# Performance work log

Hardware: AMD Instinct MI355X
Metric: run time of the kernel (lower is better)

The kernel has to match this reference:

```python
import jax, jax.numpy as jnp
import numpy as np

B, S, D, H = 4, 2048, 1024, 16
DK = D // H

def setup_inputs() -> dict:
    key = jax.random.key(0)
    ks = jax.random.split(key, 5)
    scale = 1.0 / np.sqrt(D)
    return {
        "x": jax.random.normal(ks[0], (B, S, D), dtype=jnp.float32),
        "Wq": jax.random.normal(ks[1], (H, D, DK), dtype=jnp.float32) * scale,
        "Wk": jax.random.normal(ks[2], (H, D, DK), dtype=jnp.float32) * scale,
        "Wv": jax.random.normal(ks[3], (H, D, DK), dtype=jnp.float32) * scale,
        "Wo": jax.random.normal(ks[4], (D, D), dtype=jnp.float32) * scale,
    }

def reference(x, Wq, Wk, Wv, Wo):
    # x: [B,S,D]; Wq/Wk/Wv: [H,D,DK] (stacked per-head Linear weights); Wo: [D,D]
    seq = x.shape[-2]
    q = jnp.einsum('bsd,hdk->bhsk', x, Wq)
    k = jnp.einsum('bsd,hdk->bhsk', x, Wk)
    v = jnp.einsum('bsd,hdk->bhsk', x, Wv)
    dk = q.shape[-1]
    scores = jnp.einsum('bhqk,bhsk->bhqs', q, k) / jnp.sqrt(jnp.asarray(dk, x.dtype))
    # causal mask: mask out strictly-future positions (triu, diagonal=1)
    causal = jnp.tril(jnp.ones((seq, seq), dtype=bool))  # True = keep
    scores = jnp.where(causal, scores, -jnp.inf)
    probs = jax.nn.softmax(scores, axis=-1)  # attn_pdrop = 0.0 -> dropout is identity
    attn = jnp.einsum('bhqs,bhsk->bhqk', probs, v)
    # concat heads: [B,S,H*DK]
    concat = attn.transpose(0, 2, 1, 3).reshape(x.shape[0], seq, -1)
    # output_proj: nn.Linear(D, D, bias=False) -> y = concat @ Wo.T
    return jnp.einsum('bsd,ed->bse', concat, Wo)
```

## Files before the change

kernel.cpp:

```cpp
#include <hip/hip_runtime.h>
#include <hip/hip_bf16.h>

#define B_ 4
#define S_ 2048
#define D_ 1024
#define H_ 16
#define DK_ 64

typedef __attribute__((ext_vector_type(8))) short bf16x8;
typedef __attribute__((ext_vector_type(4))) float f32x4;
typedef __attribute__((ext_vector_type(4))) unsigned int u32x4;

__device__ __forceinline__ unsigned short f2bf(float f) {
    unsigned int u = __float_as_uint(f);
    u += 0x7FFFu + ((u >> 16) & 1u);
    return (unsigned short)(u >> 16);
}

__device__ __forceinline__ unsigned int cvtpk_bf16(float lo, float hi) {
    unsigned int r;
    asm("v_cvt_pk_bf16_f32 %0, %1, %2" : "=v"(r) : "v"(lo), "v"(hi));
    return r;
}

#define BAR() do { __builtin_amdgcn_s_barrier(); asm volatile("" ::: "memory"); } while (0)

__global__ void cvt_kernel(const float* __restrict__ src, unsigned short* __restrict__ dst) {
    int i = (blockIdx.x * 256 + threadIdx.x) * 8;
    float4 f0 = *(const float4*)&src[i];
    float4 f1 = *(const float4*)&src[i + 4];
    unsigned short t[8] __attribute__((aligned(16))) = {
        f2bf(f0.x), f2bf(f0.y), f2bf(f0.z), f2bf(f0.w),
        f2bf(f1.x), f2bf(f1.y), f2bf(f1.z), f2bf(f1.w)};
    *(u32x4*)&dst[i] = *(const u32x4*)t;
}

__global__ void prepack_kernel(const float* __restrict__ Wq,
                               const float* __restrict__ Wk,
                               const float* __restrict__ Wv,
                               unsigned short* __restrict__ Wt) {
    __shared__ unsigned short Ts[64 * 65];
    int h = blockIdx.x, w3 = blockIdx.y, t = blockIdx.z;
    const float* src = (w3 == 0 ? Wq : (w3 == 1 ? Wk : Wv)) + h * D_ * DK_ + t * 64 * DK_;
    unsigned short* dst = Wt + (w3 * H_ + h) * DK_ * D_ + t * 64;
    const float wscale = (w3 == 0) ? 0.18033688011112042f : 1.0f;
    int tid = threadIdx.x;
    for (int rep = 0; rep < 16; ++rep) {
        int idx = rep * 256 + tid;
        int dl = idx >> 6, k = idx & 63;
        Ts[k * 65 + dl] = f2bf(src[dl * 64 + k] * wscale);
    }
    __syncthreads();
    for (int rep = 0; rep < 16; ++rep) {
        int idx = rep * 256 + tid;
        int kl = idx >> 6, dl = idx & 63;
        dst[kl * D_ + dl] = Ts[kl * 65 + dl];
    }
}

__global__ __launch_bounds__(256) void prep_kernel(const float* __restrict__ x,
                                                   const float* __restrict__ Wq,
                                                   const float* __restrict__ Wk,
                                                   const float* __restrict__ Wv,
                                                   const float* __restrict__ Wo,
                                                   unsigned short* __restrict__ xbf,
                                                   unsigned short* __restrict__ Wt,
                                                   unsigned short* __restrict__ Wobf) {
    __shared__ unsigned short Ts[64 * 65];
    const int bid = blockIdx.x;
    const int tid = threadIdx.x;
    if (bid < 4096 + 512) {
        const bool isx = bid < 4096;
        const float* src = isx ? x : Wo;
        unsigned short* dst = isx ? xbf : Wobf;
        int i = ((isx ? bid : bid - 4096) * 256 + tid) * 8;
        float4 f0 = *(const float4*)&src[i];
        float4 f1 = *(const float4*)&src[i + 4];
        unsigned short t[8] __attribute__((aligned(16))) = {
            f2bf(f0.x), f2bf(f0.y), f2bf(f0.z), f2bf(f0.w),
            f2bf(f1.x), f2bf(f1.y), f2bf(f1.z), f2bf(f1.w)};
        *(u32x4*)&dst[i] = *(const u32x4*)t;
    } else {
        const int pid = bid - 4608;
        const int h = pid & 15, w3 = (pid >> 4) % 3, t = pid / 48;
        const float* src = (w3 == 0 ? Wq : (w3 == 1 ? Wk : Wv)) + h * D_ * DK_ + t * 64 * DK_;
        unsigned short* dst = Wt + (w3 * H_ + h) * DK_ * D_ + t * 64;
        const float wscale = (w3 == 0) ? 0.18033688011112042f : 1.0f;
        for (int rep = 0; rep < 16; ++rep) {
            int idx = rep * 256 + tid;
            int dl = idx >> 6, k = idx & 63;
            Ts[k * 65 + dl] = f2bf(src[dl * 64 + k] * wscale);
        }
        __syncthreads();
        for (int rep = 0; rep < 16; ++rep) {
            int idx = rep * 256 + tid;
            int kl = idx >> 6, dl = idx & 63;
            dst[kl * D_ + dl] = Ts[kl * 65 + dl];
        }
    }
}

__device__ __forceinline__ void gload16(const unsigned short* gp, unsigned short* lp) {
    __builtin_amdgcn_global_load_lds((const __attribute__((address_space(1))) unsigned int*)gp,
                                     (__attribute__((address_space(3))) unsigned int*)lp,
                                     16, 0, 0);
}

__device__ __forceinline__ void stage_half(const unsigned short* __restrict__ g,
                                           unsigned short* slot, int h, int wv, int lane, int ldg) {
#pragma unroll
    for (int L = 0; L < 2; ++L) {
        int rbase = h * 128 + L * 64 + wv * 8;
        int r = rbase + (lane >> 3);
        int gc = (lane & 7) ^ ((lane >> 3) & 7);
        gload16(g + r * ldg + gc * 8, slot + rbase * 64);
    }
}

__device__ __forceinline__ void stage64_async(const unsigned short* __restrict__ g,
                                              unsigned short* lds_base, int wv, int lane, int ldg) {
#pragma unroll
    for (int it = 0; it < 2; ++it) {
        int rbase = wv * 16 + it * 8;
        int r = rbase + (lane >> 3);
        int gc = (lane & 7) ^ ((lane >> 3) & 7);
        gload16(g + r * ldg + gc * 8, lds_base + rbase * 64);
    }
}

template <bool QKV_OUT>
__global__ __launch_bounds__(512, 2) void gemm256_kernel(const unsigned short* __restrict__ A,
                                                         const unsigned short* __restrict__ Bt,
                                                         void* __restrict__ Out,
                                                         unsigned short* __restrict__ VtOut) {
    __shared__ __align__(16) unsigned short lds[65536];
    const int tid = threadIdx.x;
    const int wv = tid >> 6, lane = tid & 63, l15 = lane & 15, q4 = lane >> 4;
    const int wm = wv >> 2, wn = wv & 3;

    const int nwg = gridDim.x * gridDim.y;
    const int bid = blockIdx.x + blockIdx.y * gridDim.x;
    const int swz = (bid & 7) * (nwg >> 3) + (bid >> 3);
    const int bx = swz % gridDim.x, by = swz / gridDim.x;
    const int r0 = bx * 256, c0 = by * 256;

    const unsigned short* Ab = A + r0 * D_;
    const unsigned short* Bb = Bt + c0 * D_;

    f32x4 acc[8][4] = {};

    stage_half(Ab, lds, 0, wv, lane, D_);
    stage_half(Bb, lds + 32768, 0, wv, lane, D_);
    stage_half(Bb, lds + 32768, 1, wv, lane, D_);
    stage_half(Ab, lds, 1, wv, lane, D_);

    for (int j = 0; j < 16; ++j) {
        const bool nx = (j + 1 < 16);
        unsigned short* Ad = lds + (j & 1) * 16384;
        unsigned short* Bd = lds + 32768 + (j & 1) * 16384;
        unsigned short* An = lds + ((j + 1) & 1) * 16384;
        unsigned short* Bn = lds + 32768 + ((j + 1) & 1) * 16384;

        bf16x8 af[4][2], bfA[2][2], bfB[2][2];

        if (nx) {
            stage_half(Ab + (j + 1) * 64, An, 0, wv, lane, D_);
            asm volatile("s_waitcnt vmcnt(6)" ::: "memory");
        } else {
            asm volatile("s_waitcnt vmcnt(4)" ::: "memory");
        }
        BAR();
#pragma unroll
        for (int kk = 0; kk < 2; ++kk) {
            const int sw = ((kk * 4 + q4) ^ (l15 & 7)) * 8;
#pragma unroll
            for (int i = 0; i < 4; ++i)
                af[i][kk] = *(const bf16x8*)&Ad[(i * 32 + wm * 16 + l15) * 64 + sw];
#pragma unroll
            for (int jf = 0; jf < 2; ++jf)
                bfA[jf][kk] = *(const bf16x8*)&Bd[(jf * 64 + wn * 16 + l15) * 64 + sw];
        }
        __builtin_amdgcn_s_setprio(1);
#pragma unroll
        for (int kk = 0; kk < 2; ++kk)
#pragma unroll
            for (int i = 0; i < 4; ++i)
#pragma unroll
                for (int jf = 0; jf < 2; ++jf)
                    acc[i][jf] = __builtin_amdgcn_mfma_f32_16x16x32_bf16(af[i][kk], bfA[jf][kk], acc[i][jf], 0, 0, 0);
        __builtin_amdgcn_s_setprio(0);

        if (nx) {
            stage_half(Bb + (j + 1) * 64, Bn, 0, wv, lane, D_);
            asm volatile("s_waitcnt vmcnt(6)" ::: "memory");
        } else {
            asm volatile("s_waitcnt vmcnt(2)" ::: "memory");
        }
        BAR();
#pragma unroll
        for (int kk = 0; kk < 2; ++kk) {
            const int sw = ((kk * 4 + q4) ^ (l15 & 7)) * 8;
#pragma unroll
            for (int jf = 0; jf < 2; ++jf)
                bfB[jf][kk] = *(const bf16x8*)&Bd[((2 + jf) * 64 + wn * 16 + l15) * 64 + sw];
        }
        __builtin_amdgcn_s_setprio(1);
#pragma unroll
        for (int kk = 0; kk < 2; ++kk)
#pragma unroll
            for (int i = 0; i < 4; ++i)
#pragma unroll
                for (int jf = 0; jf < 2; ++jf)
                    acc[i][2 + jf] = __builtin_amdgcn_mfma_f32_16x16x32_bf16(af[i][kk], bfB[jf][kk], acc[i][2 + jf], 0, 0, 0);
        __builtin_amdgcn_s_setprio(0);

        if (nx) {
            stage_half(Bb + (j + 1) * 64, Bn, 1, wv, lane, D_);
            asm volatile("s_waitcnt vmcnt(6)" ::: "memory");
        } else {
            asm volatile("s_waitcnt vmcnt(0)" ::: "memory");
        }
        BAR();
#pragma unroll
        for (int kk = 0; kk < 2; ++kk) {
            const int sw = ((kk * 4 + q4) ^ (l15 & 7)) * 8;
#pragma unroll
            for (int i = 0; i < 4; ++i)
                af[i][kk] = *(const bf16x8*)&Ad[(128 + i * 32 + wm * 16 + l15) * 64 + sw];
        }
        __builtin_amdgcn_s_setprio(1);
#pragma unroll
        for (int kk = 0; kk < 2; ++kk)
#pragma unroll
            for (int i = 0; i < 4; ++i)
#pragma unroll
                for (int jf = 0; jf < 2; ++jf)
                    acc[4 + i][2 + jf] = __builtin_amdgcn_mfma_f32_16x16x32_bf16(af[i][kk], bfB[jf][kk], acc[4 + i][2 + jf], 0, 0, 0);
        __builtin_amdgcn_s_setprio(0);

        if (nx) stage_half(Ab + (j + 1) * 64, An, 1, wv, lane, D_);
        BAR();
        __builtin_amdgcn_s_setprio(1);
#pragma unroll
        for (int kk = 0; kk < 2; ++kk)
#pragma unroll
            for (int i = 0; i < 4; ++i)
#pragma unroll
                for (int jf = 0; jf < 2; ++jf)
                    acc[4 + i][jf] = __builtin_amdgcn_mfma_f32_16x16x32_bf16(af[i][kk], bfA[jf][kk], acc[4 + i][jf], 0, 0, 0);
        __builtin_amdgcn_s_setprio(0);
    }

    __syncthreads();

    if (QKV_OUT && c0 >= 2 * D_) {
        const int b = r0 >> 11, s0 = r0 & (S_ - 1);
#pragma unroll
        for (int mh = 0; mh < 2; ++mh)
#pragma unroll
            for (int ii = 0; ii < 4; ++ii)
#pragma unroll
                for (int jf = 0; jf < 4; ++jf)
#pragma unroll
                    for (int rr = 0; rr < 4; ++rr) {
                        int cl = jf * 64 + wn * 16 + l15;
                        int rl = mh * 128 + ii * 32 + wm * 16 + q4 * 4 + rr;
                        lds[cl * 256 + (rl ^ ((cl & 7) * 8))] = f2bf(acc[mh * 4 + ii][jf][rr]);
                    }
        __syncthreads();
#pragma unroll
        for (int rep = 0; rep < 16; ++rep) {
            int idx = rep * 512 + tid;
            int col = idx >> 5, ch = idx & 31;
            u32x4 v = *(const u32x4*)&lds[col * 256 + ((ch * 8) ^ ((col & 7) * 8))];
            int gcol = c0 + col;
            int vrow = b * 1024 + (gcol & 1023);
            *(u32x4*)&VtOut[vrow * S_ + s0 + ch * 8] = v;
        }
    } else {
#pragma unroll
        for (int mh = 0; mh < 2; ++mh)
#pragma unroll
            for (int ii = 0; ii < 4; ++ii)
#pragma unroll
                for (int jf = 0; jf < 4; ++jf)
#pragma unroll
                    for (int rr = 0; rr < 4; ++rr) {
                        int grow = r0 + mh * 128 + ii * 32 + wm * 16 + q4 * 4 + rr;
                        int gcol = c0 + jf * 64 + wn * 16 + l15;
                        if (QKV_OUT) {
                            int bb = grow >> 11, s = grow & (S_ - 1);
                            int w3 = gcol >> 10, h = (gcol >> 6) & 15, dk = gcol & 63;
                            ((unsigned short*)Out)[(((w3 * B_ + bb) * H_ + h) * S_ + s) * DK_ + dk] =
                                f2bf(acc[mh * 4 + ii][jf][rr]);
                        } else {
                            ((float*)Out)[grow * D_ + gcol] = acc[mh * 4 + ii][jf][rr];
                        }
                    }
    }
}

__global__ __launch_bounds__(256) void attn_kernel(const unsigned short* __restrict__ qkv,
                                                   unsigned short* __restrict__ concat) {
    static const int J[16] = {15, 13, 11, 9, 0, 2, 4, 6, 14, 12, 10, 8, 1, 3, 5, 7};
    const int bh = blockIdx.x;
    const int b = bh >> 4, h = bh & 15;
    const int j = J[blockIdx.y];
    const int q0 = j * 128;
    const int nk = 2 * j + 2;

    const unsigned short* Qp = qkv + ((0 * B_ + b) * H_ + h) * S_ * DK_;
    const unsigned short* Kp = qkv + ((1 * B_ + b) * H_ + h) * S_ * DK_;
    const unsigned short* Vt = qkv + 2 * B_ * H_ * S_ * DK_ + (b * H_ + h) * DK_ * S_;

    __shared__ __align__(16) unsigned short Kb[3][64 * 64];
    __shared__ __align__(16) unsigned short Vb[3][64 * 64];

    const int tid = threadIdx.x;
    const int wv = tid >> 6, lane = tid & 63, l15 = lane & 15, q4 = lane >> 4;

    bf16x8 aq[2][2];
#pragma unroll
    for (int rt = 0; rt < 2; ++rt)
#pragma unroll
        for (int kk = 0; kk < 2; ++kk)
            aq[rt][kk] = *(const bf16x8*)&Qp[(q0 + wv * 32 + rt * 16 + l15) * DK_ + kk * 32 + q4 * 8];

    __syncthreads();

    stage64_async(Kp, Kb[0], wv, lane, DK_);
    stage64_async(Vt, Vb[0], wv, lane, S_);
    stage64_async(Kp + 64 * DK_, Kb[1], wv, lane, DK_);
    stage64_async(Vt + 64, Vb[1], wv, lane, S_);

    f32x4 o[2][4] = {};
    float l_[2] = {0.0f, 0.0f};

    for (int t = 0; t < nk; ++t) {
        if (t + 1 < nk) asm volatile("s_waitcnt vmcnt(4)" ::: "memory");
        else            asm volatile("s_waitcnt vmcnt(0)" ::: "memory");
        BAR();

        if (t + 2 < nk) {
            const int k2 = (t + 2) * 64;
            stage64_async(Kp + k2 * DK_, Kb[(t + 2) % 3], wv, lane, DK_);
            stage64_async(Vt + k2, Vb[(t + 2) % 3], wv, lane, S_);
        }
        const unsigned short* Kt = Kb[t % 3];
        const unsigned short* Vtt = Vb[t % 3];
        const int k0 = t * 64;

        if ((t + 1 < nk) || (wv >= 2)) {
            f32x4 sa[2][4] = {};
            __builtin_amdgcn_s_setprio(1);
#pragma unroll
            for (int kk = 0; kk < 2; ++kk) {
                const int sw = ((kk * 4 + q4) ^ (l15 & 7)) * 8;
#pragma unroll
                for (int ct = 0; ct < 4; ++ct) {
                    bf16x8 bk = *(const bf16x8*)&Kt[(ct * 16 + l15) * 64 + sw];
                    sa[0][ct] = __builtin_amdgcn_mfma_f32_16x16x32_bf16(bk, aq[0][kk], sa[0][ct], 0, 0, 0);
                    sa[1][ct] = __builtin_amdgcn_mfma_f32_16x16x32_bf16(bk, aq[1][kk], sa[1][ct], 0, 0, 0);
                }
            }
            __builtin_amdgcn_s_setprio(0);

            if (t < nk - 2) {
#pragma unroll
                for (int rt = 0; rt < 2; ++rt)
#pragma unroll
                    for (int ct = 0; ct < 4; ++ct)
#pragma unroll
                        for (int r = 0; r < 4; ++r)
                            sa[rt][ct][r] = __builtin_amdgcn_exp2f(sa[rt][ct][r]);
            } else {
                const int kb = k0 + q4 * 4;
#pragma unroll
                for (int rt = 0; rt < 2; ++rt) {
                    const int qrow = q0 + wv * 32 + rt * 16 + l15;
#pragma unroll
                    for (int ct = 0; ct < 4; ++ct)
#pragma unroll
                        for (int r = 0; r < 4; ++r) {
                            float e = __builtin_amdgcn_exp2f(sa[rt][ct][r]);
                            sa[rt][ct][r] = (kb + ct * 16 + r <= qrow) ? e : 0.0f;
                        }
                }
            }

#pragma unroll
            for (int rt = 0; rt < 2; ++rt)
#pragma unroll
                for (int ct = 0; ct < 4; ++ct)
                    l_[rt] += (sa[rt][ct][0] + sa[rt][ct][1]) + (sa[rt][ct][2] + sa[rt][ct][3]);

            bf16x8 F[2][2];
#pragma unroll
            for (int rt = 0; rt < 2; ++rt)
#pragma unroll
                for (int kk = 0; kk < 2; ++kk) {
                    u32x4 w;
#pragma unroll
                    for (int u = 0; u < 2; ++u) {
                        unsigned int a = cvtpk_bf16(sa[rt][2 * kk][2 * u], sa[rt][2 * kk][2 * u + 1]);
                        unsigned int c = cvtpk_bf16(sa[rt][2 * kk + 1][2 * u], sa[rt][2 * kk + 1][2 * u + 1]);
                        asm("v_permlane32_swap_b32 %0, %1" : "+v"(a), "+v"(c));
                        asm("v_permlane16_swap_b32 %0, %1" : "+v"(a), "+v"(c));
                        w[u] = a;
                        w[2 + u] = c;
                    }
                    F[rt][kk] = *(const bf16x8*)&w;
                }

            __builtin_amdgcn_s_setprio(1);
#pragma unroll
            for (int kk = 0; kk < 2; ++kk) {
                const int sw = ((kk * 4 + q4) ^ (l15 & 7)) * 8;
#pragma unroll
                for (int cd = 0; cd < 4; ++cd) {
                    bf16x8 bv = *(const bf16x8*)&Vtt[(cd * 16 + l15) * 64 + sw];
                    o[0][cd] = __builtin_amdgcn_mfma_f32_16x16x32_bf16(F[0][kk], bv, o[0][cd], 0, 0, 0);
                    o[1][cd] = __builtin_amdgcn_mfma_f32_16x16x32_bf16(F[1][kk], bv, o[1][cd], 0, 0, 0);
                }
            }
            __builtin_amdgcn_s_setprio(0);
        }
    }

#pragma unroll
    for (int rt = 0; rt < 2; ++rt) {
        float lr = l_[rt];
        lr += __shfl_xor(lr, 16);
        lr += __shfl_xor(lr, 32);
#pragma unroll
        for (int r = 0; r < 4; ++r) {
            float lfull = __shfl(lr, (lane & 48) | (q4 * 4 + r));
            float inv = 1.0f / fmaxf(lfull, 1.0e-37f);
            int row = q0 + wv * 32 + rt * 16 + q4 * 4 + r;
#pragma unroll
            for (int cd = 0; cd < 4; ++cd) {
                int col = h * DK_ + cd * 16 + l15;
                concat[(b * S_ + row) * D_ + col] = f2bf(o[rt][cd][r] * inv);
            }
        }
    }
}

extern "C" void kernel_launch(void* const* d_in, const int* in_sizes, int n_in,
                              void* d_out, int out_size, void* d_ws, size_t ws_size,
                              hipStream_t stream) {
    const float* x  = (const float*)d_in[0];
    const float* Wq = (const float*)d_in[1];
    const float* Wk = (const float*)d_in[2];
    const float* Wv = (const float*)d_in[3];
    const float* Wo = (const float*)d_in[4];

    unsigned short* qkv    = (unsigned short*)d_ws;
    unsigned short* Wt     = qkv + 3 * B_ * H_ * S_ * DK_;
    unsigned short* xbf    = Wt + 3 * H_ * DK_ * D_;
    unsigned short* concat = xbf;
    unsigned short* VtOut  = qkv + 2 * B_ * H_ * S_ * DK_;

    const size_t need_shorts = (size_t)3 * B_ * H_ * S_ * DK_ + 3 * H_ * DK_ * D_ + B_ * S_ * D_ + D_ * D_;
    const bool sep = ws_size >= need_shorts * sizeof(unsigned short);

    if (sep) {
        unsigned short* Wobf = xbf + B_ * S_ * D_;
        prep_kernel<<<4096 + 512 + 768, 256, 0, stream>>>(x, Wq, Wk, Wv, Wo, xbf, Wt, Wobf);
        gemm256_kernel<true><<<dim3(32, 12), 512, 0, stream>>>(xbf, Wt, qkv, VtOut);
        attn_kernel<<<dim3(64, 16), 256, 0, stream>>>(qkv, concat);
        gemm256_kernel<false><<<dim3(32, 4), 512, 0, stream>>>(concat, Wobf, d_out, nullptr);
    } else {
        unsigned short* Wobf = Wt;
        cvt_kernel<<<B_ * S_ * D_ / 2048, 256, 0, stream>>>(x, xbf);
        prepack_kernel<<<dim3(H_, 3, 16), 256, 0, stream>>>(Wq, Wk, Wv, Wt);
        gemm256_kernel<true><<<dim3(32, 12), 512, 0, stream>>>(xbf, Wt, qkv, VtOut);
        cvt_kernel<<<D_ * D_ / 2048, 256, 0, stream>>>(Wo, Wobf);
        attn_kernel<<<dim3(64, 16), 256, 0, stream>>>(qkv, concat);
        gemm256_kernel<false><<<dim3(32, 4), 512, 0, stream>>>(concat, Wobf, d_out, nullptr);
    }
}
```

Measured before the change: 250.8 us.

## Use 128x256 tiled GEMM for output projection to fill more CUs

Adds a new gemm128 kernel with 128x256 tiles, 8 waves, and a four-phase pipelined schedule that stages A and B halves asynchronously between MFMA phases. It replaces the 256x256-tile kernel for the output projection, doubling the workgroup count from 128 to 256 so that more of the GPU's compute units get work. The cost is more total reloading of B tiles and a new hand-tuned vmcnt and barrier schedule that could be fragile.

```diff
diff --git a/kernel.cpp b/kernel.cpp
--- a/kernel.cpp
+++ b/kernel.cpp
@@ -117,6 +117,24 @@
     }
 }
 
+__device__ __forceinline__ void stageA_half(const unsigned short* __restrict__ g,
+                                            unsigned short* lds_base, int wv, int lane, int ldg) {
+    int r = wv * 8 + (lane >> 3);
+    int gc = (lane & 7) ^ ((lane >> 3) & 7);
+    gload16(g + r * ldg + gc * 8, lds_base + (wv * 8) * 64);
+}
+
+__device__ __forceinline__ void stageB_half(const unsigned short* __restrict__ g,
+                                            unsigned short* lds_base, int wv, int lane, int ldg) {
+#pragma unroll
+    for (int L = 0; L < 2; ++L) {
+        int rbase = wv * 16 + L * 8;
+        int r = rbase + (lane >> 3);
+        int gc = (lane & 7) ^ ((lane >> 3) & 7);
+        gload16(g + r * ldg + gc * 8, lds_base + rbase * 64);
+    }
+}
+
 __device__ __forceinline__ void stage64_async(const unsigned short* __restrict__ g,
                                               unsigned short* lds_base, int wv, int lane, int ldg) {
 #pragma unroll
@@ -300,6 +318,110 @@
     }
 }
 
+template <int MH, int NH>
+__device__ __forceinline__ void phase_mfma(const unsigned short* Asl, const unsigned short* Bsl,
+                                           int db, int wm, int wn, int l15, int q4,
+                                           f32x4 (&acc)[2][2][2][2]) {
+    bf16x8 af[2][2], bf[2][2];
+#pragma unroll
+    for (int kk = 0; kk < 2; ++kk) {
+        const int sw = ((kk * 4 + q4) ^ (l15 & 7)) * 8;
+#pragma unroll
+        for (int m4 = 0; m4 < 2; ++m4)
+            af[m4][kk] = *(const bf16x8*)&Asl[(db + MH) * 4096 + (wm * 32 + m4 * 16 + l15) * 64 + sw];
+#pragma unroll
+        for (int n2 = 0; n2 < 2; ++n2)
+            bf[n2][kk] = *(const bf16x8*)&Bsl[(db + NH) * 8192 + (wn * 32 + n2 * 16 + l15) * 64 + sw];
+    }
+    __builtin_amdgcn_s_setprio(1);
+#pragma unroll
+    for (int kk = 0; kk < 2; ++kk)
+#pragma unroll
+        for (int m4 = 0; m4 < 2; ++m4)
+#pragma unroll
+            for (int n2 = 0; n2 < 2; ++n2)
+                acc[MH][NH][m4][n2] =
+                    __builtin_amdgcn_mfma_f32_16x16x32_bf16(af[m4][kk], bf[n2][kk], acc[MH][NH][m4][n2], 0, 0, 0);
+    __builtin_amdgcn_s_setprio(0);
+}
+
+__global__ __launch_bounds__(512) void gemm128_kernel(const unsigned short* __restrict__ A,
+                                                      const unsigned short* __restrict__ Bt,
+                                                      float* __restrict__ Out) {
+    __shared__ __align__(16) unsigned short lds[49152];
+    unsigned short* Asl = lds;
+    unsigned short* Bsl = lds + 16384;
+
+    const int tid = threadIdx.x;
+    const int wv = tid >> 6, lane = tid & 63, l15 = lane & 15, q4 = lane >> 4;
+    const int wm = wv >> 2, wn = wv & 3;
+
+    const int nwg = gridDim.x * gridDim.y;
+    const int bid = blockIdx.x + blockIdx.y * gridDim.x;
+    const int swz = (bid & 7) * (nwg >> 3) + (bid >> 3);
+    const int bx = swz % gridDim.x, by = swz / gridDim.x;
+    const int r0 = bx * 128, c0 = by * 256;
+
+    const unsigned short* Ab = A + r0 * D_;
+    const unsigned short* Bb = Bt + c0 * D_;
+
+    f32x4 acc[2][2][2][2] = {};
+
+    stageA_half(Ab, Asl, wv, lane, D_);
+    stageB_half(Bb, Bsl, wv, lane, D_);
+    stageB_half(Bb + 128 * D_, Bsl + 8192, wv, lane, D_);
+
+    for (int j = 0; j < 16; ++j) {
+        const int db = (j & 1) * 2;
+        const int ndb = ((j + 1) & 1) * 2;
+        const bool nx = (j + 1 < 16);
+
+        stageA_half(Ab + 64 * D_ + j * 64, Asl + (db + 1) * 4096, wv, lane, D_);
+        asm volatile("s_waitcnt vmcnt(3)" ::: "memory");
+        BAR();
+        phase_mfma<0, 0>(Asl, Bsl, db, wm, wn, l15, q4, acc);
+
+        if (nx) {
+            stageA_half(Ab + (j + 1) * 64, Asl + (ndb + 0) * 4096, wv, lane, D_);
+            asm volatile("s_waitcnt vmcnt(2)" ::: "memory");
+        } else {
+            asm volatile("s_waitcnt vmcnt(1)" ::: "memory");
+        }
+        BAR();
+        phase_mfma<0, 1>(Asl, Bsl, db, wm, wn, l15, q4, acc);
+
+        if (nx) {
+            stageB_half(Bb + (j + 1) * 64, Bsl + (ndb + 0) * 8192, wv, lane, D_);
+            asm volatile("s_waitcnt vmcnt(3)" ::: "memory");
+        } else {
+            asm volatile("s_waitcnt vmcnt(0)" ::: "memory");
+        }
+        BAR();
+        phase_mfma<1, 1>(Asl, Bsl, db, wm, wn, l15, q4, acc);
+
+        if (nx) stageB_half(Bb + 128 * D_ + (j + 1) * 64, Bsl + (ndb + 1) * 8192, wv, lane, D_);
+        BAR();
+        phase_mfma<1, 0>(Asl, Bsl, db, wm, wn, l15, q4, acc);
+    }
+
+    __syncthreads();
+
+#pragma unroll
+    for (int mh = 0; mh < 2; ++mh)
+#pragma unroll
+        for (int nh = 0; nh < 2; ++nh)
+#pragma unroll
+            for (int m4 = 0; m4 < 2; ++m4)
+#pragma unroll
+                for (int n2 = 0; n2 < 2; ++n2)
+#pragma unroll
+                    for (int rr = 0; rr < 4; ++rr) {
+                        int grow = r0 + mh * 64 + wm * 32 + m4 * 16 + q4 * 4 + rr;
+                        int gcol = c0 + nh * 128 + wn * 32 + n2 * 16 + l15;
+                        Out[grow * D_ + gcol] = acc[mh][nh][m4][n2][rr];
+                    }
+}
+
 __global__ __launch_bounds__(256) void attn_kernel(const unsigned short* __restrict__ qkv,
                                                    unsigned short* __restrict__ concat) {
     static const int J[16] = {15, 13, 11, 9, 0, 2, 4, 6, 14, 12, 10, 8, 1, 3, 5, 7};
@@ -469,7 +591,7 @@
         prep_kernel<<<4096 + 512 + 768, 256, 0, stream>>>(x, Wq, Wk, Wv, Wo, xbf, Wt, Wobf);
         gemm256_kernel<true><<<dim3(32, 12), 512, 0, stream>>>(xbf, Wt, qkv, VtOut);
         attn_kernel<<<dim3(64, 16), 256, 0, stream>>>(qkv, concat);
-        gemm256_kernel<false><<<dim3(32, 4), 512, 0, stream>>>(concat, Wobf, d_out, nullptr);
+        gemm128_kernel<<<dim3(64, 4), 512, 0, stream>>>(concat, Wobf, (float*)d_out);
     } else {
         unsigned short* Wobf = Wt;
         cvt_kernel<<<B_ * S_ * D_ / 2048, 256, 0, stream>>>(x, xbf);
@@ -477,6 +599,6 @@
         gemm256_kernel<true><<<dim3(32, 12), 512, 0, stream>>>(xbf, Wt, qkv, VtOut);
         cvt_kernel<<<D_ * D_ / 2048, 256, 0, stream>>>(Wo, Wobf);
         attn_kernel<<<dim3(64, 16), 256, 0, stream>>>(qkv, concat);
-        gemm256_kernel<false><<<dim3(32, 4), 512, 0, stream>>>(concat, Wobf, d_out, nullptr);
-    }
-}
+        gemm128_kernel<<<dim3(64, 4), 512, 0, stream>>>(concat, Wobf, (float*)d_out);
+    }
+}
```

Measured after the change: 246.6 us. No clear change (-1.7%).
